# Performance work log

Measured on AMD Instinct MI355X. Metric: run time of the kernel, lower is better.

The kernel has to match this reference:

```python
import jax, jax.numpy as jnp
import numpy as np

NUM_LEVELS = 6
LEVEL_DIM = 4
LOG2_HASHMAP = 19
HASHMAP_SIZE = 1 << LOG2_HASHMAP
BASE_RES = 16
DESIRED_RES = 512
SPHERE_RADIUS = 500.0
N_RAYS = 1048576
PER_LEVEL_SCALE = float(np.exp(np.log(DESIRED_RES / BASE_RES) / (NUM_LEVELS - 1)))  # = 2.0
PRIMES = (1, 2654435761, 805459861)
# static 8 trilinear corner offsets [8,3]
_CORNERS_NP = np.array([[i, j, k] for i in (0, 1) for j in (0, 1) for k in (0, 1)], dtype=np.int64)


def _level_params(level):
    # torch-ngp / Instant-NGP convention: scale = base * gamma**L - 1, res = ceil(scale)+1
    scale = BASE_RES * (PER_LEVEL_SCALE ** level) - 1.0
    res = int(np.ceil(scale)) + 1
    return scale, res


def hash_grid_encode(coords, table):
    """coords: [N,3] in [0,1]; table: [L, HASHMAP_SIZE, D] -> [N, L*D]."""
    corners_f = jnp.asarray(_CORNERS_NP, dtype=coords.dtype)        # [8,3]
    corners_u = jnp.asarray(_CORNERS_NP, dtype=jnp.uint32)          # [8,3]
    outs = []
    for level in range(NUM_LEVELS):
        scale, res = _level_params(level)
        pos = coords * scale + 0.5                                   # [N,3]
        pos_grid = jnp.floor(pos)
        frac = pos - pos_grid                                        # [N,3] in [0,1)
        pg = pos_grid.astype(jnp.uint32)                             # [N,3]
        cg = pg[:, None, :] + corners_u[None, :, :]                  # [N,8,3]
        if res ** 3 <= HASHMAP_SIZE:
            # dense indexing for coarse levels
            cg = jnp.minimum(cg, jnp.uint32(res - 1))
            idx = cg[..., 0] + cg[..., 1] * jnp.uint32(res) + cg[..., 2] * jnp.uint32(res * res)
        else:
            # spatial hash with xor of primes, table size is a power of two
            h = (cg[..., 0] * jnp.uint32(PRIMES[0])
                 ^ cg[..., 1] * jnp.uint32(PRIMES[1])
                 ^ cg[..., 2] * jnp.uint32(PRIMES[2]))
            idx = h & jnp.uint32(HASHMAP_SIZE - 1)
        feats = table[level][idx.astype(jnp.int32)]                  # [N,8,D] gather
        # trilinear weights: prod over dims of (frac if corner==1 else 1-frac)
        w = jnp.prod(jnp.where(corners_f[None] == 1.0, frac[:, None, :], 1.0 - frac[:, None, :]), axis=-1)  # [N,8]
        outs.append(jnp.sum(feats * w[..., None], axis=1))           # [N,D]
    return jnp.concatenate(outs, axis=-1)                            # [N, L*D]


def setup_inputs() -> dict:
    key = jax.random.key(0)
    k1, k2, k3 = jax.random.split(key, 3)
    view_dirs = jax.random.normal(k1, (N_RAYS, 3), dtype=jnp.float32)
    view_dirs = view_dirs / jnp.linalg.norm(view_dirs, axis=-1, keepdims=True)
    ray_origins = jax.random.normal(k2, (N_RAYS, 3), dtype=jnp.float32)  # cameras near origin, radius >> extent
    table = jax.random.uniform(k3, (NUM_LEVELS, HASHMAP_SIZE, LEVEL_DIM),
                               dtype=jnp.float32, minval=-0.1, maxval=0.1)
    return {"view_dirs": view_dirs, "ray_origins": ray_origins, "table": table}


def reference(view_dirs, ray_origins, table):
    # ray-sphere intersection (a=1 since dirs normalized)
    b = 2.0 * jnp.sum(ray_origins * view_dirs, axis=-1, keepdims=True)
    c = jnp.sum(ray_origins * ray_origins, axis=-1, keepdims=True) - SPHERE_RADIUS ** 2
    disc = b * b - 4.0 * c
    t = (-b + jnp.sqrt(jnp.maximum(disc, 0.0))) / 2.0
    pts = ray_origins + t * view_dirs                                 # [N,3]
    coords = jnp.clip((pts + SPHERE_RADIUS) / (2.0 * SPHERE_RADIUS), 0.0, 1.0)
    return hash_grid_encode(coords, table)                            # [N, 24]
```

## Files before the change

kernel.cpp:

```cpp
#include <hip/hip_runtime.h>

constexpr unsigned kHashmapSize = 1u << 19;
constexpr float kSphereR = 500.0f;
constexpr int kLog2Buckets = 15;
constexpr int kNumBuckets = 1 << kLog2Buckets;

typedef float v4f __attribute__((ext_vector_type(4)));

__device__ __forceinline__ unsigned part1by2(unsigned x) {
    x &= 0x3FFu;
    x = (x | (x << 16)) & 0x030000FFu;
    x = (x | (x << 8))  & 0x0300F00Fu;
    x = (x | (x << 4))  & 0x030C30C3u;
    x = (x | (x << 2))  & 0x09249249u;
    return x;
}

__device__ __forceinline__ void ray_coords(const float* __restrict__ dirs,
                                           const float* __restrict__ orig,
                                           int n, float& cx, float& cy, float& cz) {
    float dx = dirs[3 * n + 0], dy = dirs[3 * n + 1], dz = dirs[3 * n + 2];
    float ox = orig[3 * n + 0], oy = orig[3 * n + 1], oz = orig[3 * n + 2];
    float b = 2.0f * ((ox * dx + oy * dy) + oz * dz);
    float c = ((ox * ox + oy * oy) + oz * oz) - kSphereR * kSphereR;
    float disc = b * b - 4.0f * c;
    float t = (-b + sqrtf(fmaxf(disc, 0.0f))) * 0.5f;
    float px = ox + t * dx, py = oy + t * dy, pz = oz + t * dz;
    cx = fminf(fmaxf((px + kSphereR) / (2.0f * kSphereR), 0.0f), 1.0f);
    cy = fminf(fmaxf((py + kSphereR) / (2.0f * kSphereR), 0.0f), 1.0f);
    cz = fminf(fmaxf((pz + kSphereR) / (2.0f * kSphereR), 0.0f), 1.0f);
}

__device__ __forceinline__ unsigned bucket_of(float cx, float cy, float cz) {
    unsigned qx = min(31u, (unsigned)(cx * 32.0f));
    unsigned qy = min(31u, (unsigned)(cy * 32.0f));
    unsigned qz = min(31u, (unsigned)(cz * 32.0f));
    return part1by2(qx) | (part1by2(qy) << 1) | (part1by2(qz) << 2);
}

__global__ __launch_bounds__(256)
void zero_hist_kernel(unsigned* __restrict__ hist) {
    int i = blockIdx.x * 256 + threadIdx.x;
    if (i < kNumBuckets) hist[i] = 0u;
}

__global__ __launch_bounds__(256)
void hist_kernel(const float* __restrict__ dirs, const float* __restrict__ orig,
                 unsigned* __restrict__ hist, int n_rays) {
    int n = blockIdx.x * 256 + threadIdx.x;
    if (n >= n_rays) return;
    float cx, cy, cz;
    ray_coords(dirs, orig, n, cx, cy, cz);
    atomicAdd(&hist[bucket_of(cx, cy, cz)], 1u);
}

__global__ __launch_bounds__(1024)
void scan_kernel(unsigned* __restrict__ hist) {
    __shared__ unsigned sums[1024];
    const int t = threadIdx.x;
    constexpr int kPer = kNumBuckets / 1024;
    unsigned local[kPer];
    unsigned s = 0;
#pragma unroll
    for (int i = 0; i < kPer; ++i) { local[i] = hist[t * kPer + i]; s += local[i]; }
    sums[t] = s;
    __syncthreads();
    for (int off = 1; off < 1024; off <<= 1) {
        unsigned v = (t >= off) ? sums[t - off] : 0u;
        __syncthreads();
        sums[t] += v;
        __syncthreads();
    }
    unsigned run = (t == 0) ? 0u : sums[t - 1];
#pragma unroll
    for (int i = 0; i < kPer; ++i) { unsigned c = local[i]; hist[t * kPer + i] = run; run += c; }
}

__global__ __launch_bounds__(256)
void scatter_kernel(const float* __restrict__ dirs, const float* __restrict__ orig,
                    unsigned* __restrict__ offs, v4f* __restrict__ sorted, int n_rays) {
    int n = blockIdx.x * 256 + threadIdx.x;
    if (n >= n_rays) return;
    float cx, cy, cz;
    ray_coords(dirs, orig, n, cx, cy, cz);
    unsigned key = bucket_of(cx, cy, cz);
    unsigned pos = atomicAdd(&offs[key], 1u);
    v4f v; v.x = cx; v.y = cy; v.z = cz; v.w = __uint_as_float((unsigned)n);
    sorted[pos] = v;
}

__global__ __launch_bounds__(256)
void encode_kernel(const v4f* __restrict__ sorted,
                   const float4* __restrict__ table4,
                   float* __restrict__ out,
                   int n_rays, int nblocks) {
    int bid = blockIdx.x;
    int chunk = nblocks >> 3;
    int swz = (bid & 7) * chunk + (bid >> 3);
    int i = swz * 256 + (int)threadIdx.x;
    if (i >= n_rays) return;

    v4f s = sorted[i];
    float cx = s.x, cy = s.y, cz = s.z;
    unsigned rayid = __float_as_uint(s.w);

    constexpr float kScale[6] = {15.f, 31.f, 63.f, 127.f, 255.f, 511.f};
    constexpr unsigned kRes[6] = {16u, 32u, 64u, 128u, 256u, 512u};

    float* outp = out + (size_t)rayid * 24;

#pragma unroll
    for (int L = 0; L < 6; ++L) {
        const float sc = kScale[L];
        const unsigned res = kRes[L];
        const bool dense = (L < 3);

        float posx = cx * sc + 0.5f;
        float posy = cy * sc + 0.5f;
        float posz = cz * sc + 0.5f;
        float gx_f = floorf(posx), gy_f = floorf(posy), gz_f = floorf(posz);
        float fx = posx - gx_f, fy = posy - gy_f, fz = posz - gz_f;
        unsigned gx = (unsigned)gx_f, gy = (unsigned)gy_f, gz = (unsigned)gz_f;

        const float4* __restrict__ tl = table4 + (size_t)L * kHashmapSize;

        unsigned idx[8];
#pragma unroll
        for (int cr = 0; cr < 8; ++cr) {
            unsigned ii = (unsigned)(cr >> 2);
            unsigned jj = (unsigned)((cr >> 1) & 1);
            unsigned kk = (unsigned)(cr & 1);
            unsigned x = gx + ii, y = gy + jj, z = gz + kk;
            if (dense) {
                x = min(x, res - 1u);
                y = min(y, res - 1u);
                z = min(z, res - 1u);
                idx[cr] = x + y * res + z * res * res;
            } else {
                idx[cr] = (x * 1u ^ y * 2654435761u ^ z * 805459861u) & (kHashmapSize - 1u);
            }
        }

        float4 f[8];
#pragma unroll
        for (int cr = 0; cr < 8; ++cr) f[cr] = tl[idx[cr]];

        float wx[2] = {1.0f - fx, fx};
        float wy[2] = {1.0f - fy, fy};
        float wz[2] = {1.0f - fz, fz};

        float4 acc = make_float4(0.f, 0.f, 0.f, 0.f);
#pragma unroll
        for (int cr = 0; cr < 8; ++cr) {
            float w = (wx[(cr >> 2) & 1] * wy[(cr >> 1) & 1]) * wz[cr & 1];
            acc.x += f[cr].x * w;
            acc.y += f[cr].y * w;
            acc.z += f[cr].z * w;
            acc.w += f[cr].w * w;
        }

        *(float4*)(outp + L * 4) = acc;
    }
}

extern "C" void kernel_launch(void* const* d_in, const int* in_sizes, int n_in,
                              void* d_out, int out_size, void* d_ws, size_t ws_size,
                              hipStream_t stream) {
    const float* dirs = (const float*)d_in[0];
    const float* orig = (const float*)d_in[1];
    const float4* table4 = (const float4*)d_in[2];
    float* out = (float*)d_out;

    int n_rays = in_sizes[0] / 3;

    v4f* sorted = (v4f*)d_ws;
    unsigned* hist = (unsigned*)((char*)d_ws + (size_t)n_rays * 16);

    const int block = 256;
    int grid = (n_rays + block - 1) / block;

    zero_hist_kernel<<<(kNumBuckets + 255) / 256, block, 0, stream>>>(hist);
    hist_kernel<<<grid, block, 0, stream>>>(dirs, orig, hist, n_rays);
    scan_kernel<<<1, 1024, 0, stream>>>(hist);
    scatter_kernel<<<grid, block, 0, stream>>>(dirs, orig, hist, sorted, n_rays);
    encode_kernel<<<grid, block, 0, stream>>>(sorted, table4, out, n_rays, grid);
}
```

Before: 410.5 us.

## Record per-ray ranks in histogram pass, prefetch next level gathers, nontemporal I/O

The histogram pass now saves each ray's atomic rank, so the scatter pass computes its destination as bucket base plus rank and no longer needs a second round of contended atomics. The encode kernel software-pipelines the levels by issuing the eight table gathers for the next level before it interpolates the current one, which hides gather latency. It also uses nontemporal loads for the sorted rays and nontemporal stores for the output. The costs are a 4 MB auxiliary rank buffer and higher register pressure from holding two levels of gathered features, which could reduce occupancy.

Result: slower. 533.9 us (+30.1%).

```diff
diff --git a/kernel.cpp b/kernel.cpp
--- a/kernel.cpp
+++ b/kernel.cpp
@@ -2,8 +2,7 @@
 
 constexpr unsigned kHashmapSize = 1u << 19;
 constexpr float kSphereR = 500.0f;
-constexpr int kLog2Buckets = 15;
-constexpr int kNumBuckets = 1 << kLog2Buckets;
+constexpr int kNumBuckets = 1 << 15;
 
 typedef float v4f __attribute__((ext_vector_type(4)));
 
@@ -45,13 +44,13 @@
 }
 
 __global__ __launch_bounds__(256)
-void hist_kernel(const float* __restrict__ dirs, const float* __restrict__ orig,
-                 unsigned* __restrict__ hist, int n_rays) {
+void rank_kernel(const float* __restrict__ dirs, const float* __restrict__ orig,
+                 unsigned* __restrict__ hist, unsigned* __restrict__ aux, int n_rays) {
     int n = blockIdx.x * 256 + threadIdx.x;
     if (n >= n_rays) return;
     float cx, cy, cz;
     ray_coords(dirs, orig, n, cx, cy, cz);
-    atomicAdd(&hist[bucket_of(cx, cy, cz)], 1u);
+    aux[n] = atomicAdd(&hist[bucket_of(cx, cy, cz)], 1u);
 }
 
 __global__ __launch_bounds__(1024)
@@ -77,21 +76,50 @@
 }
 
 __global__ __launch_bounds__(256)
-void scatter_kernel(const float* __restrict__ dirs, const float* __restrict__ orig,
-                    unsigned* __restrict__ offs, v4f* __restrict__ sorted, int n_rays) {
+void place_kernel(const float* __restrict__ dirs, const float* __restrict__ orig,
+                  const unsigned* __restrict__ base, const unsigned* __restrict__ aux,
+                  v4f* __restrict__ sorted, int n_rays) {
     int n = blockIdx.x * 256 + threadIdx.x;
     if (n >= n_rays) return;
     float cx, cy, cz;
     ray_coords(dirs, orig, n, cx, cy, cz);
     unsigned key = bucket_of(cx, cy, cz);
-    unsigned pos = atomicAdd(&offs[key], 1u);
+    unsigned pos = base[key] + aux[n];
     v4f v; v.x = cx; v.y = cy; v.z = cz; v.w = __uint_as_float((unsigned)n);
     sorted[pos] = v;
 }
 
+__device__ __forceinline__ void level_setup(int L, float cx, float cy, float cz,
+                                            unsigned idx[8], float& fx, float& fy, float& fz) {
+    const float sc = (float)(16 << L) - 1.0f;
+    const unsigned res = 16u << L;
+    const bool dense = (L < 3);
+    float posx = cx * sc + 0.5f;
+    float posy = cy * sc + 0.5f;
+    float posz = cz * sc + 0.5f;
+    float gx_f = floorf(posx), gy_f = floorf(posy), gz_f = floorf(posz);
+    fx = posx - gx_f; fy = posy - gy_f; fz = posz - gz_f;
+    unsigned gx = (unsigned)gx_f, gy = (unsigned)gy_f, gz = (unsigned)gz_f;
+#pragma unroll
+    for (int cr = 0; cr < 8; ++cr) {
+        unsigned ii = (unsigned)(cr >> 2);
+        unsigned jj = (unsigned)((cr >> 1) & 1);
+        unsigned kk = (unsigned)(cr & 1);
+        unsigned x = gx + ii, y = gy + jj, z = gz + kk;
+        if (dense) {
+            x = min(x, res - 1u);
+            y = min(y, res - 1u);
+            z = min(z, res - 1u);
+            idx[cr] = x + y * res + z * res * res;
+        } else {
+            idx[cr] = (x * 1u ^ y * 2654435761u ^ z * 805459861u) & (kHashmapSize - 1u);
+        }
+    }
+}
+
 __global__ __launch_bounds__(256)
 void encode_kernel(const v4f* __restrict__ sorted,
-                   const float4* __restrict__ table4,
+                   const v4f* __restrict__ table4,
                    float* __restrict__ out,
                    int n_rays, int nblocks) {
     int bid = blockIdx.x;
@@ -100,66 +128,47 @@
     int i = swz * 256 + (int)threadIdx.x;
     if (i >= n_rays) return;
 
-    v4f s = sorted[i];
+    v4f s = __builtin_nontemporal_load(&sorted[i]);
     float cx = s.x, cy = s.y, cz = s.z;
     unsigned rayid = __float_as_uint(s.w);
+    float* outp = out + (size_t)rayid * 24;
 
-    constexpr float kScale[6] = {15.f, 31.f, 63.f, 127.f, 255.f, 511.f};
-    constexpr unsigned kRes[6] = {16u, 32u, 64u, 128u, 256u, 512u};
-
-    float* outp = out + (size_t)rayid * 24;
+    unsigned idx[8];
+    float fx, fy, fz;
+    level_setup(0, cx, cy, cz, idx, fx, fy, fz);
+    v4f fcur[8];
+    {
+        const v4f* __restrict__ tl = table4;
+#pragma unroll
+        for (int cr = 0; cr < 8; ++cr) fcur[cr] = tl[idx[cr]];
+    }
 
 #pragma unroll
     for (int L = 0; L < 6; ++L) {
-        const float sc = kScale[L];
-        const unsigned res = kRes[L];
-        const bool dense = (L < 3);
-
-        float posx = cx * sc + 0.5f;
-        float posy = cy * sc + 0.5f;
-        float posz = cz * sc + 0.5f;
-        float gx_f = floorf(posx), gy_f = floorf(posy), gz_f = floorf(posz);
-        float fx = posx - gx_f, fy = posy - gy_f, fz = posz - gz_f;
-        unsigned gx = (unsigned)gx_f, gy = (unsigned)gy_f, gz = (unsigned)gz_f;
-
-        const float4* __restrict__ tl = table4 + (size_t)L * kHashmapSize;
-
-        unsigned idx[8];
+        v4f fnxt[8];
+        float fxn = 0.f, fyn = 0.f, fzn = 0.f;
+        if (L < 5) {
+            unsigned idxn[8];
+            level_setup(L + 1, cx, cy, cz, idxn, fxn, fyn, fzn);
+            const v4f* __restrict__ tl = table4 + (size_t)(L + 1) * kHashmapSize;
 #pragma unroll
-        for (int cr = 0; cr < 8; ++cr) {
-            unsigned ii = (unsigned)(cr >> 2);
-            unsigned jj = (unsigned)((cr >> 1) & 1);
-            unsigned kk = (unsigned)(cr & 1);
-            unsigned x = gx + ii, y = gy + jj, z = gz + kk;
-            if (dense) {
-                x = min(x, res - 1u);
-                y = min(y, res - 1u);
-                z = min(z, res - 1u);
-                idx[cr] = x + y * res + z * res * res;
-            } else {
-                idx[cr] = (x * 1u ^ y * 2654435761u ^ z * 805459861u) & (kHashmapSize - 1u);
-            }
+            for (int cr = 0; cr < 8; ++cr) fnxt[cr] = tl[idxn[cr]];
         }
-
-        float4 f[8];
-#pragma unroll
-        for (int cr = 0; cr < 8; ++cr) f[cr] = tl[idx[cr]];
 
         float wx[2] = {1.0f - fx, fx};
         float wy[2] = {1.0f - fy, fy};
         float wz[2] = {1.0f - fz, fz};
-
-        float4 acc = make_float4(0.f, 0.f, 0.f, 0.f);
+        v4f acc; acc.x = 0.f; acc.y = 0.f; acc.z = 0.f; acc.w = 0.f;
 #pragma unroll
         for (int cr = 0; cr < 8; ++cr) {
             float w = (wx[(cr >> 2) & 1] * wy[(cr >> 1) & 1]) * wz[cr & 1];
-            acc.x += f[cr].x * w;
-            acc.y += f[cr].y * w;
-            acc.z += f[cr].z * w;
-            acc.w += f[cr].w * w;
+            acc += fcur[cr] * w;
         }
+        __builtin_nontemporal_store(acc, (v4f*)(outp + L * 4));
 
-        *(float4*)(outp + L * 4) = acc;
+        fx = fxn; fy = fyn; fz = fzn;
+#pragma unroll
+        for (int cr = 0; cr < 8; ++cr) fcur[cr] = fnxt[cr];
     }
 }
 
@@ -168,20 +177,21 @@
                               hipStream_t stream) {
     const float* dirs = (const float*)d_in[0];
     const float* orig = (const float*)d_in[1];
-    const float4* table4 = (const float4*)d_in[2];
+    const v4f* table4 = (const v4f*)d_in[2];
     float* out = (float*)d_out;
 
     int n_rays = in_sizes[0] / 3;
 
     v4f* sorted = (v4f*)d_ws;
     unsigned* hist = (unsigned*)((char*)d_ws + (size_t)n_rays * 16);
+    unsigned* aux = hist + kNumBuckets;
 
     const int block = 256;
     int grid = (n_rays + block - 1) / block;
 
     zero_hist_kernel<<<(kNumBuckets + 255) / 256, block, 0, stream>>>(hist);
-    hist_kernel<<<grid, block, 0, stream>>>(dirs, orig, hist, n_rays);
+    rank_kernel<<<grid, block, 0, stream>>>(dirs, orig, hist, aux, n_rays);
     scan_kernel<<<1, 1024, 0, stream>>>(hist);
-    scatter_kernel<<<grid, block, 0, stream>>>(dirs, orig, hist, sorted, n_rays);
+    place_kernel<<<grid, block, 0, stream>>>(dirs, orig, hist, aux, sorted, n_rays);
     encode_kernel<<<grid, block, 0, stream>>>(sorted, table4, out, n_rays, grid);
 }
```
